# Kernel optimization log

Hardware: AMD Instinct MI355X
Metric: run time of the kernel (lower is better)

The kernel has to match this reference:

```python
import jax, jax.numpy as jnp
import numpy as np
from jax import lax

TOPK = 5
MAX_CANDIDATES = 32
MAX_LAG_CAP = 168


def setup_inputs() -> dict:
    key = jax.random.key(0)
    x = jax.random.normal(key, (32, 4096, 512), dtype=jnp.float32)
    return {"x": x}


def reference(x):
    B, L, D = x.shape
    x_mean = x.mean(axis=-1)                          # [B, L]
    max_lag = min(L - 1, MAX_LAG_CAP)
    num = min(max_lag, MAX_CANDIDATES)
    # torch.linspace(..., dtype=long) truncates toward zero; astype does too
    lags = jnp.linspace(1.0, float(max_lag), num).astype(jnp.int32)  # [num]

    t = jnp.arange(L)

    def score_for_lag(lag):
        # (x_mean[:, :-lag] * x_mean[:, lag:]).mean(1), via masked circular shift
        shifted = jnp.roll(x_mean, -lag, axis=1)       # x_mean[:, t+lag] (wrapped)
        mask = (t < (L - lag)).astype(x_mean.dtype)    # [L]
        return (x_mean * shifted * mask).sum(axis=1) / (L - lag).astype(x_mean.dtype)

    scores = jax.vmap(score_for_lag, out_axes=1)(lags)  # [B, num]

    k = min(TOPK, num)
    vals, idx = lax.top_k(scores, k)                    # [B, k]
    sel_lags = lags[idx]                                # [B, k] int
    weights = vals / (vals.sum(axis=1, keepdims=True) + 1e-6)  # [B, k]

    roll_batch = jax.vmap(lambda xb, lag: jnp.roll(xb, lag, axis=0))

    out = jnp.zeros_like(x)
    for j in range(k):  # small fixed k
        rolled = roll_batch(x, sel_lags[:, j])          # [B, L, D]
        out = out + weights[:, j, None, None] * rolled
    return out
```

## Files before the change

kernel.cpp:

```cpp
#include <hip/hip_runtime.h>

#define BB 32
#define LL 4096
#define DD 512
#define NUM 32
#define KK 5

typedef float f32x4 __attribute__((ext_vector_type(4)));

__device__ __constant__ int d_LAGS[NUM] = {
    1, 6, 11, 17, 22, 27, 33, 38, 44, 49, 54, 60, 65, 71, 76, 81,
    87, 92, 97, 103, 108, 114, 119, 124, 130, 135, 141, 146, 151, 157, 162, 168};

__global__ __launch_bounds__(256) void k_mean(const float* __restrict__ x,
                                              float* __restrict__ xm) {
    int row  = blockIdx.x * 4 + (threadIdx.x >> 6);
    int lane = threadIdx.x & 63;
    const float* p = x + (size_t)row * DD;
    f32x4 a = *reinterpret_cast<const f32x4*>(p + 4 * lane);
    f32x4 b = *reinterpret_cast<const f32x4*>(p + 4 * lane + 256);
    float s = (a.x + a.y) + (a.z + a.w) + (b.x + b.y) + (b.z + b.w);
#pragma unroll
    for (int off = 32; off > 0; off >>= 1) s += __shfl_down(s, off, 64);
    if (lane == 0) xm[row] = s * (1.0f / DD);
}

__global__ __launch_bounds__(256) void k_scores(const float* __restrict__ xm,
                                                float* __restrict__ scores) {
    int b   = blockIdx.x >> 5;
    int k   = blockIdx.x & 31;
    int lag = d_LAGS[k];
    const float* row = xm + b * LL;
    int n = LL - lag;
    float s = 0.0f;
    for (int t = threadIdx.x; t < n; t += 256) s += row[t] * row[t + lag];
#pragma unroll
    for (int off = 32; off > 0; off >>= 1) s += __shfl_down(s, off, 64);
    __shared__ float red[4];
    int wid = threadIdx.x >> 6, lane = threadIdx.x & 63;
    if (lane == 0) red[wid] = s;
    __syncthreads();
    if (threadIdx.x == 0) {
        float tot = (red[0] + red[1]) + (red[2] + red[3]);
        scores[blockIdx.x] = tot / (float)n;
    }
}

__global__ __launch_bounds__(64) void k_topk(const float* __restrict__ scores,
                                             float* __restrict__ w,
                                             int* __restrict__ sel) {
    int b = threadIdx.x;
    if (b >= BB) return;
    float sc[NUM];
#pragma unroll
    for (int i = 0; i < NUM; i++) sc[i] = scores[b * NUM + i];
    float vals[KK];
    int idx[KK];
#pragma unroll
    for (int j = 0; j < KK; j++) {
        float best = -INFINITY;
        int bi = 0;
#pragma unroll
        for (int i = 0; i < NUM; i++) {
            if (sc[i] > best) { best = sc[i]; bi = i; }
        }
        vals[j] = best;
        idx[j]  = bi;
        sc[bi]  = -INFINITY;
    }
    float sum = 0.0f;
#pragma unroll
    for (int j = 0; j < KK; j++) sum += vals[j];
    float den = sum + 1e-6f;
#pragma unroll
    for (int j = 0; j < KK; j++) {
        w[b * KK + j]   = vals[j] / den;
        sel[b * KK + j] = d_LAGS[idx[j]];
    }
}

__global__ __launch_bounds__(256) void k_combine(const float* __restrict__ x,
                                                 const float* __restrict__ w,
                                                 const int* __restrict__ sel,
                                                 float* __restrict__ out) {
    unsigned bid = blockIdx.x;
    const unsigned PAIRS_PER_XCD = (BB * LL / 2) / 8;
    unsigned pid = (bid & 7u) * PAIRS_PER_XCD + (bid >> 3);
    unsigned r   = pid * 2 + (threadIdx.x >> 7);
    int b = (int)(r >> 12);
    int t = (int)(r & 4095u);

    __shared__ float ww[KK];
    __shared__ int   llag[KK];
    if (threadIdx.x < KK) {
        ww[threadIdx.x]   = w[b * KK + threadIdx.x];
        llag[threadIdx.x] = sel[b * KK + threadIdx.x];
    }
    __syncthreads();

    const float* xb = x + (size_t)b * (LL * DD);
    int d4 = threadIdx.x & 127;
    f32x4 acc = {0.f, 0.f, 0.f, 0.f};
#pragma unroll
    for (int j = 0; j < KK; j++) {
        int src = (t - llag[j]) & (LL - 1);
        f32x4 v = *reinterpret_cast<const f32x4*>(xb + (size_t)src * DD + 4 * d4);
        float wj = ww[j];
        acc.x += wj * v.x;
        acc.y += wj * v.y;
        acc.z += wj * v.z;
        acc.w += wj * v.w;
    }
    __builtin_nontemporal_store(acc,
        reinterpret_cast<f32x4*>(out + (size_t)r * DD + 4 * d4));
}

extern "C" void kernel_launch(void* const* d_in, const int* in_sizes, int n_in,
                              void* d_out, int out_size, void* d_ws, size_t ws_size,
                              hipStream_t stream) {
    const float* x = (const float*)d_in[0];
    float* out = (float*)d_out;

    char* ws = (char*)d_ws;
    float* xm     = (float*)(ws);
    float* scores = (float*)(ws + (size_t)BB * LL * 4);
    float* wts    = (float*)(ws + (size_t)BB * LL * 4 + BB * NUM * 4);
    int*   sel    = (int*)  (ws + (size_t)BB * LL * 4 + BB * NUM * 4 + BB * KK * 4);

    k_mean<<<(BB * LL) / 4, 256, 0, stream>>>(x, xm);
    k_scores<<<BB * NUM, 256, 0, stream>>>(xm, scores);
    k_topk<<<1, 64, 0, stream>>>(scores, wts, sel);
    k_combine<<<(BB * LL) / 2, 256, 0, stream>>>(x, wts, sel, out);
}
```

Measured before the change: 134.3 us.

## Fuse score and top-k kernels, widen combine blocks to four rows

Merges the autocorrelation score and top-k kernels into one kernel per batch. It stages each row's means in shared memory and has each wavefront compute eight lags, which removes one launch and the global scores round trip. The combine kernel now uses 512-thread blocks covering four rows, and each thread loads the weights and lags directly instead of going through shared memory with a barrier. In exchange, the score stage runs on only 32 blocks, which may underuse the GPU, and it adds redundant scalar loads in combine.

```diff
diff --git a/kernel.cpp b/kernel.cpp
--- a/kernel.cpp
+++ b/kernel.cpp
@@ -25,85 +25,84 @@
     if (lane == 0) xm[row] = s * (1.0f / DD);
 }
 
-__global__ __launch_bounds__(256) void k_scores(const float* __restrict__ xm,
-                                                float* __restrict__ scores) {
-    int b   = blockIdx.x >> 5;
-    int k   = blockIdx.x & 31;
-    int lag = d_LAGS[k];
-    const float* row = xm + b * LL;
-    int n = LL - lag;
-    float s = 0.0f;
-    for (int t = threadIdx.x; t < n; t += 256) s += row[t] * row[t + lag];
+__global__ __launch_bounds__(256) void k_scores_topk(const float* __restrict__ xm,
+                                                     float* __restrict__ w,
+                                                     int* __restrict__ sel) {
+    __shared__ float row[LL];
+    __shared__ float sc[NUM];
+    int b = blockIdx.x;
+    for (int i = threadIdx.x; i < LL; i += 256) row[i] = xm[b * LL + i];
+    __syncthreads();
+
+    int wid = threadIdx.x >> 6, lane = threadIdx.x & 63;
 #pragma unroll
-    for (int off = 32; off > 0; off >>= 1) s += __shfl_down(s, off, 64);
-    __shared__ float red[4];
-    int wid = threadIdx.x >> 6, lane = threadIdx.x & 63;
-    if (lane == 0) red[wid] = s;
+    for (int q = 0; q < 8; ++q) {
+        int k   = q * 4 + wid;
+        int lag = d_LAGS[k];
+        int n   = LL - lag;
+        float s = 0.0f;
+        for (int t = lane; t < n; t += 64) s += row[t] * row[t + lag];
+#pragma unroll
+        for (int off = 32; off > 0; off >>= 1) s += __shfl_down(s, off, 64);
+        if (lane == 0) sc[k] = s / (float)n;
+    }
     __syncthreads();
+
     if (threadIdx.x == 0) {
-        float tot = (red[0] + red[1]) + (red[2] + red[3]);
-        scores[blockIdx.x] = tot / (float)n;
+        float v[NUM];
+#pragma unroll
+        for (int i = 0; i < NUM; i++) v[i] = sc[i];
+        float vals[KK];
+        int   idx[KK];
+#pragma unroll
+        for (int j = 0; j < KK; j++) {
+            float best = -INFINITY;
+            int bi = 0;
+#pragma unroll
+            for (int i = 0; i < NUM; i++) {
+                if (v[i] > best) { best = v[i]; bi = i; }
+            }
+            vals[j] = best;
+            idx[j]  = bi;
+            v[bi]   = -INFINITY;
+        }
+        float sum = 0.0f;
+#pragma unroll
+        for (int j = 0; j < KK; j++) sum += vals[j];
+        float den = sum + 1e-6f;
+#pragma unroll
+        for (int j = 0; j < KK; j++) {
+            w[b * KK + j]   = vals[j] / den;
+            sel[b * KK + j] = d_LAGS[idx[j]];
+        }
     }
 }
 
-__global__ __launch_bounds__(64) void k_topk(const float* __restrict__ scores,
-                                             float* __restrict__ w,
-                                             int* __restrict__ sel) {
-    int b = threadIdx.x;
-    if (b >= BB) return;
-    float sc[NUM];
-#pragma unroll
-    for (int i = 0; i < NUM; i++) sc[i] = scores[b * NUM + i];
-    float vals[KK];
-    int idx[KK];
-#pragma unroll
-    for (int j = 0; j < KK; j++) {
-        float best = -INFINITY;
-        int bi = 0;
-#pragma unroll
-        for (int i = 0; i < NUM; i++) {
-            if (sc[i] > best) { best = sc[i]; bi = i; }
-        }
-        vals[j] = best;
-        idx[j]  = bi;
-        sc[bi]  = -INFINITY;
-    }
-    float sum = 0.0f;
-#pragma unroll
-    for (int j = 0; j < KK; j++) sum += vals[j];
-    float den = sum + 1e-6f;
-#pragma unroll
-    for (int j = 0; j < KK; j++) {
-        w[b * KK + j]   = vals[j] / den;
-        sel[b * KK + j] = d_LAGS[idx[j]];
-    }
-}
-
-__global__ __launch_bounds__(256) void k_combine(const float* __restrict__ x,
+__global__ __launch_bounds__(512) void k_combine(const float* __restrict__ x,
                                                  const float* __restrict__ w,
                                                  const int* __restrict__ sel,
                                                  float* __restrict__ out) {
     unsigned bid = blockIdx.x;
-    const unsigned PAIRS_PER_XCD = (BB * LL / 2) / 8;
-    unsigned pid = (bid & 7u) * PAIRS_PER_XCD + (bid >> 3);
-    unsigned r   = pid * 2 + (threadIdx.x >> 7);
+    const unsigned QUADS_PER_XCD = (BB * LL / 4) / 8;
+    unsigned qid = (bid & 7u) * QUADS_PER_XCD + (bid >> 3);
+    unsigned r   = qid * 4 + (threadIdx.x >> 7);
     int b = (int)(r >> 12);
     int t = (int)(r & 4095u);
 
-    __shared__ float ww[KK];
-    __shared__ int   llag[KK];
-    if (threadIdx.x < KK) {
-        ww[threadIdx.x]   = w[b * KK + threadIdx.x];
-        llag[threadIdx.x] = sel[b * KK + threadIdx.x];
+    float ww[KK];
+    int   lg[KK];
+#pragma unroll
+    for (int j = 0; j < KK; j++) {
+        ww[j] = w[b * KK + j];
+        lg[j] = sel[b * KK + j];
     }
-    __syncthreads();
 
     const float* xb = x + (size_t)b * (LL * DD);
     int d4 = threadIdx.x & 127;
     f32x4 acc = {0.f, 0.f, 0.f, 0.f};
 #pragma unroll
     for (int j = 0; j < KK; j++) {
-        int src = (t - llag[j]) & (LL - 1);
+        int src = (t - lg[j]) & (LL - 1);
         f32x4 v = *reinterpret_cast<const f32x4*>(xb + (size_t)src * DD + 4 * d4);
         float wj = ww[j];
         acc.x += wj * v.x;
@@ -122,13 +121,11 @@
     float* out = (float*)d_out;
 
     char* ws = (char*)d_ws;
-    float* xm     = (float*)(ws);
-    float* scores = (float*)(ws + (size_t)BB * LL * 4);
-    float* wts    = (float*)(ws + (size_t)BB * LL * 4 + BB * NUM * 4);
-    int*   sel    = (int*)  (ws + (size_t)BB * LL * 4 + BB * NUM * 4 + BB * KK * 4);
+    float* xm  = (float*)(ws);
+    float* wts = (float*)(ws + (size_t)BB * LL * 4);
+    int*   sel = (int*)  (ws + (size_t)BB * LL * 4 + BB * KK * 4);
 
     k_mean<<<(BB * LL) / 4, 256, 0, stream>>>(x, xm);
-    k_scores<<<BB * NUM, 256, 0, stream>>>(xm, scores);
-    k_topk<<<1, 64, 0, stream>>>(scores, wts, sel);
-    k_combine<<<(BB * LL) / 2, 256, 0, stream>>>(x, wts, sel, out);
+    k_scores_topk<<<BB, 256, 0, stream>>>(xm, wts, sel);
+    k_combine<<<(BB * LL) / 4, 512, 0, stream>>>(x, wts, sel, out);
 }
```

Result: slower. 155.7 us (+16.0%).
